# Performance work log

Hardware: AMD Instinct MI355X
Metric: run time of the kernel (lower is better)

The kernel has to match this reference:

```python
import jax, jax.numpy as jnp
import numpy as np

B, C, L = 32, 8, 2048
K, S = 512, 64  # num_shapelets, shapelets_size


def setup_inputs() -> dict:
    key = jax.random.key(0)
    k1, k2 = jax.random.split(key)
    x = jax.random.normal(k1, (B, C, L), dtype=jnp.float32)
    shapelets = jax.random.normal(k2, (C, K, S), dtype=jnp.float32)
    return {"x": x, "shapelets": shapelets}


def reference(x, shapelets):
    # x: [B, C, L]; shapelets: [C, K, S]
    s = shapelets.shape[-1]
    n_dims = x.shape[1]
    W = x.shape[2] - s + 1  # number of sliding windows
    # unfold(2, S, 1): gather overlapping windows -> [B, C, W, S]
    idx = jnp.arange(W)[:, None] + jnp.arange(s)[None, :]
    xw = x[:, :, idx]
    # L2-normalize windows along window length (clamp min like torch)
    xw = xw / jnp.maximum(jnp.linalg.norm(xw, axis=-1, keepdims=True), 1e-8)
    # L2-normalize shapelets along length
    sn = shapelets / jnp.maximum(jnp.linalg.norm(shapelets, axis=-1, keepdims=True), 1e-8)
    # matmul [B,C,W,S] @ [C,S,K] then sum over C, fused into one einsum -> [B, W, K]
    sim = jnp.einsum('bcws,cks->bwk', xw, sn) / n_dims
    sim = jax.nn.relu(sim)
    # max over window positions -> [B, K]; keep the singleton channel dim like torch ([B,1,K])
    out = jnp.max(sim, axis=1)
    return out[:, None, :]
```

## Files before the change

### kernel.cpp

```cpp
#include <hip/hip_runtime.h>


#define B_ 32
#define C_ 8
#define L_ 2048
#define K_ 512
#define S_ 64
#define W_ 1985
#define XS_ 2176

typedef _Float16 f16x8  __attribute__((ext_vector_type(8)));
typedef _Float16 f16x8u __attribute__((ext_vector_type(8), aligned(4)));
typedef float    f32x16 __attribute__((ext_vector_type(16)));

__global__ __launch_bounds__(256)
void prep_k(const float* __restrict__ x, const float* __restrict__ sh,
            _Float16* __restrict__ Bp, float* __restrict__ invn,
            _Float16* __restrict__ xh0, _Float16* __restrict__ xh1,
            float* __restrict__ out) {
    __shared__ float xr[L_];
    const int tid = threadIdx.x;
    const int blk = blockIdx.x;

    if (blk < 128) {
        const int sb   = blk * 4 + (tid >> 6);
        const int c    = sb >> 6;
        const int kq   = (sb >> 4) & 3;
        const int nt   = sb & 15;
        const int lane = tid & 63;
        const int half = lane >> 5;
        const int q    = nt * 32 + (lane & 31);

        const float4* sp = (const float4*)(sh + (size_t)(c * K_ + q) * S_);
        float ss = 0.f;
        #pragma unroll
        for (int i = 0; i < 8; ++i) {
            float4 v = sp[half * 8 + i];
            ss += v.x * v.x + v.y * v.y + v.z * v.z + v.w * v.w;
        }
        ss += __shfl_xor(ss, 32);
        float inv = 1.f / fmaxf(sqrtf(ss), 1e-8f);

        float4 u0 = sp[kq * 4 + half * 2];
        float4 u1 = sp[kq * 4 + half * 2 + 1];
        f16x8 o;
        o[0] = (_Float16)(u0.x * inv); o[1] = (_Float16)(u0.y * inv);
        o[2] = (_Float16)(u0.z * inv); o[3] = (_Float16)(u0.w * inv);
        o[4] = (_Float16)(u1.x * inv); o[5] = (_Float16)(u1.y * inv);
        o[6] = (_Float16)(u1.z * inv); o[7] = (_Float16)(u1.w * inv);
        ((f16x8*)Bp)[((c * 4 + kq) * 16 + nt) * 64 + lane] = o;
    } else {
        const int r = blk - 128;
        const float* xp = x + (size_t)r * L_;
        for (int i = tid; i < L_ / 4; i += 256)
            ((float4*)xr)[i] = ((const float4*)xp)[i];
        __syncthreads();

        float* ivp = invn + (size_t)r * L_;
        const int w0 = tid * 8;
        float ss = 0.f;
        if (w0 < W_) {
            #pragma unroll
            for (int j = 0; j < S_; ++j) { float v = xr[w0 + j]; ss += v * v; }
        }
        #pragma unroll
        for (int u = 0; u < 8; ++u) {
            int w = w0 + u;
            float o = 0.f;
            if (u > 0 && w < W_)
                ss += xr[w + 63] * xr[w + 63] - xr[w - 1] * xr[w - 1];
            if (w < W_) o = 0.125f / fmaxf(sqrtf(ss), 1e-8f);
            if (w < L_) ivp[w] = o;
        }

        _Float16* p0 = xh0 + (size_t)r * XS_;
        _Float16* p1 = xh1 + (size_t)r * XS_;
        for (int i = tid; i < XS_ / 8; i += 256) {
            f16x8 o0, o1;
            #pragma unroll
            for (int j = 0; j < 8; ++j) {
                int e = i * 8 + j;
                o0[j] = (_Float16)((e     < L_) ? xr[e]     : 0.f);
                o1[j] = (_Float16)((e + 1 < L_) ? xr[e + 1] : 0.f);
            }
            ((f16x8*)p0)[i] = o0;
            ((f16x8*)p1)[i] = o1;
        }
        if (r < 64) out[r * 256 + tid] = 0.f;
    }
}

__device__ __forceinline__ void load_c(
    int c, const f16x8* __restrict__ bpbase, const _Float16* __restrict__ xbase,
    const float* __restrict__ ivbase, int m0, int m1,
    f16x8 (&bf)[8], f16x8 (&ar)[8], float (&iv)[2])
{
    iv[0] = ivbase[(size_t)c * L_ + m0];
    iv[1] = ivbase[(size_t)c * L_ + m1];
    #pragma unroll
    for (int ks = 0; ks < 4; ++ks)
        #pragma unroll
        for (int nt = 0; nt < 2; ++nt)
            bf[ks * 2 + nt] = bpbase[((c * 4 + ks) * 16 + nt) * 64];
    const _Float16* xp = xbase + (size_t)c * XS_;
    #pragma unroll
    for (int mt = 0; mt < 2; ++mt)
        #pragma unroll
        for (int ks = 0; ks < 4; ++ks)
            ar[mt * 4 + ks] = *(const f16x8u*)(xp + mt * 32 + ks * 16);
}

__device__ __forceinline__ void comp_c(
    const f16x8 (&bf)[8], const f16x8 (&ar)[8], const float (&iv)[2],
    f32x16 (&acc)[2][2])
{
    const _Float16 h0 = (_Float16)iv[0], h1 = (_Float16)iv[1];
    f16x8 is0, is1;
    #pragma unroll
    for (int j = 0; j < 8; ++j) { is0[j] = h0; is1[j] = h1; }
    #pragma unroll
    for (int ks = 0; ks < 4; ++ks) {
        f16x8 a0 = ar[0 * 4 + ks] * is0;
        f16x8 a1 = ar[1 * 4 + ks] * is1;
        #pragma unroll
        for (int nt = 0; nt < 2; ++nt) {
            acc[0][nt] = __builtin_amdgcn_mfma_f32_32x32x16_f16(
                a0, bf[ks * 2 + nt], acc[0][nt], 0, 0, 0);
            acc[1][nt] = __builtin_amdgcn_mfma_f32_32x32x16_f16(
                a1, bf[ks * 2 + nt], acc[1][nt], 0, 0, 0);
        }
    }
}

__global__ __launch_bounds__(256, 2)
void mcs_k(const _Float16* __restrict__ xh0, const _Float16* __restrict__ xh1,
           const _Float16* __restrict__ Bp, const float* __restrict__ invn,
           float* __restrict__ out) {
    const int wt  = blockIdx.x;
    const int ng  = blockIdx.y;
    const int b   = blockIdx.z;
    const int tid = threadIdx.x;
    const int lane = tid & 63;
    const int wv   = tid >> 6;
    const int mg   = wv >> 1;
    const int nw   = wv & 1;

    const int l31 = lane & 31;
    const int lh  = lane >> 5;
    const int Wb  = wt * 128 + mg * 64;
    const int m0  = Wb + l31;
    const int m1  = Wb + 32 + l31;

    const _Float16* xb = (l31 & 1) ? (xh1 - 1) : xh0;
    const _Float16* xbase = xb + (size_t)b * C_ * XS_ + Wb + l31 + lh * 8;
    const float*   ivbase = invn + (size_t)b * C_ * L_;
    const f16x8*   bpbase = (const f16x8*)Bp + (ng * 4 + nw * 2) * 64 + lane;

    f32x16 acc[2][2];
    #pragma unroll
    for (int mt = 0; mt < 2; ++mt)
        #pragma unroll
        for (int nt = 0; nt < 2; ++nt)
            #pragma unroll
            for (int r = 0; r < 16; ++r) acc[mt][nt][r] = 0.f;

    f16x8 bA[8], aA[8], bB[8], aB[8];
    float ivA[2], ivB[2];

    load_c(0, bpbase, xbase, ivbase, m0, m1, bA, aA, ivA);
    #pragma unroll 1
    for (int cp = 0; cp < 4; ++cp) {
        const int c0 = cp * 2;
        load_c(c0 + 1, bpbase, xbase, ivbase, m0, m1, bB, aB, ivB);
        comp_c(bA, aA, ivA, acc);
        if (cp < 3)
            load_c(c0 + 2, bpbase, xbase, ivbase, m0, m1, bA, aA, ivA);
        comp_c(bB, aB, ivB, acc);
    }

    float m[2];
    #pragma unroll
    for (int nt = 0; nt < 2; ++nt) {
        float v = 0.f;
        #pragma unroll
        for (int mt = 0; mt < 2; ++mt)
            #pragma unroll
            for (int r = 0; r < 16; ++r) v = fmaxf(v, acc[mt][nt][r]);
        v = fmaxf(v, __shfl_xor(v, 32));
        m[nt] = v;
    }

    __shared__ float red[2][2][32];
    if (mg == 0 && lane < 32) {
        red[nw][0][l31] = m[0];
        red[nw][1][l31] = m[1];
    }
    __syncthreads();
    if (mg == 1 && lane < 32) {
        #pragma unroll
        for (int nt = 0; nt < 2; ++nt) {
            float v = fmaxf(m[nt], red[nw][nt][l31]);
            atomicMax((unsigned int*)(out + (size_t)b * K_ + ng * 128 + nw * 64 + nt * 32 + l31),
                      __float_as_uint(v));
        }
    }
}

extern "C" void kernel_launch(void* const* d_in, const int* in_sizes, int n_in,
                              void* d_out, int out_size, void* d_ws, size_t ws_size,
                              hipStream_t stream) {
    const float* x  = (const float*)d_in[0];
    const float* sh = (const float*)d_in[1];
    float* out = (float*)d_out;

    _Float16* Bp   = (_Float16*)d_ws;
    float*    invn = (float*)((char*)d_ws + (512 << 10));
    _Float16* xh0  = (_Float16*)((char*)d_ws + (512 << 10) + (2 << 20));
    _Float16* xh1  = xh0 + (size_t)B_ * C_ * XS_;

    prep_k<<<dim3(384), dim3(256), 0, stream>>>(x, sh, Bp, invn, xh0, xh1, out);
    mcs_k<<<dim3(16, 4, B_), dim3(256), 0, stream>>>(xh0, xh1, Bp, invn, out);
}
```

Baseline: 104.0 us.

## Stage shapelet fragments into LDS via direct global-to-LDS loads shared across waves

Shapelet B fragments for each channel are no longer loaded per wave straight into registers. Each wave now issues 16-byte global_load_lds copies for one quarter of the fragments into a double-buffered shared array. All waves then read their B operands from LDS, so the two M-groups no longer fetch the same data from global memory twice, and B register pressure drops. The cost is two block-wide barriers per channel pair and extra LDS reads. Correctness depends on the barrier waiting for the asynchronous LDS writes to finish.

```diff
diff --git a/kernel.cpp b/kernel.cpp
--- a/kernel.cpp
+++ b/kernel.cpp
@@ -90,18 +90,18 @@
     }
 }
 
-__device__ __forceinline__ void load_c(
-    int c, const f16x8* __restrict__ bpbase, const _Float16* __restrict__ xbase,
-    const float* __restrict__ ivbase, int m0, int m1,
-    f16x8 (&bf)[8], f16x8 (&ar)[8], float (&iv)[2])
+__device__ __forceinline__ void glds16(const void* g, void* l) {
+    __builtin_amdgcn_global_load_lds(
+        (const __attribute__((address_space(1))) unsigned int*)g,
+        (__attribute__((address_space(3))) unsigned int*)l, 16, 0, 0);
+}
+
+__device__ __forceinline__ void loadA(
+    int c, const _Float16* __restrict__ xbase, const float* __restrict__ ivbase,
+    int m0, int m1, f16x8 (&ar)[8], float (&iv)[2])
 {
     iv[0] = ivbase[(size_t)c * L_ + m0];
     iv[1] = ivbase[(size_t)c * L_ + m1];
-    #pragma unroll
-    for (int ks = 0; ks < 4; ++ks)
-        #pragma unroll
-        for (int nt = 0; nt < 2; ++nt)
-            bf[ks * 2 + nt] = bpbase[((c * 4 + ks) * 16 + nt) * 64];
     const _Float16* xp = xbase + (size_t)c * XS_;
     #pragma unroll
     for (int mt = 0; mt < 2; ++mt)
@@ -110,14 +110,22 @@
             ar[mt * 4 + ks] = *(const f16x8u*)(xp + mt * 32 + ks * 16);
 }
 
-__device__ __forceinline__ void comp_c(
-    const f16x8 (&bf)[8], const f16x8 (&ar)[8], const float (&iv)[2],
-    f32x16 (&acc)[2][2])
+__device__ __forceinline__ void compC(
+    const f16x8* __restrict__ bsl, int lane, int nw,
+    const f16x8 (&ar)[8], const float (&iv)[2], f32x16 (&acc)[2][2])
 {
+    f16x8 bf[8];
+    #pragma unroll
+    for (int ks = 0; ks < 4; ++ks)
+        #pragma unroll
+        for (int nt = 0; nt < 2; ++nt)
+            bf[ks * 2 + nt] = bsl[(ks * 4 + nw * 2 + nt) * 64 + lane];
+
     const _Float16 h0 = (_Float16)iv[0], h1 = (_Float16)iv[1];
     f16x8 is0, is1;
     #pragma unroll
     for (int j = 0; j < 8; ++j) { is0[j] = h0; is1[j] = h1; }
+
     #pragma unroll
     for (int ks = 0; ks < 4; ++ks) {
         f16x8 a0 = ar[0 * 4 + ks] * is0;
@@ -151,10 +159,13 @@
     const int m0  = Wb + l31;
     const int m1  = Wb + 32 + l31;
 
+    __shared__ f16x8 Bs[2][16][64];
+    __shared__ float red[2][2][32];
+
     const _Float16* xb = (l31 & 1) ? (xh1 - 1) : xh0;
     const _Float16* xbase = xb + (size_t)b * C_ * XS_ + Wb + l31 + lh * 8;
     const float*   ivbase = invn + (size_t)b * C_ * L_;
-    const f16x8*   bpbase = (const f16x8*)Bp + (ng * 4 + nw * 2) * 64 + lane;
+    const f16x8*   sg = (const f16x8*)Bp + ((wv * 16 + ng * 4) * 64) + lane;
 
     f32x16 acc[2][2];
     #pragma unroll
@@ -164,19 +175,33 @@
             #pragma unroll
             for (int r = 0; r < 16; ++r) acc[mt][nt][r] = 0.f;
 
-    f16x8 bA[8], aA[8], bB[8], aB[8];
+    f16x8 aA[8], aB[8];
     float ivA[2], ivB[2];
 
-    load_c(0, bpbase, xbase, ivbase, m0, m1, bA, aA, ivA);
+    #define STAGE(c, buf)                                              \
+        { _Pragma("unroll")                                            \
+          for (int u = 0; u < 4; ++u)                                  \
+              glds16(sg + ((c) * 64 + u) * 64, &Bs[buf][wv * 4 + u][0]); }
+
+    STAGE(0, 0);
+    loadA(0, xbase, ivbase, m0, m1, aA, ivA);
+    __syncthreads();
+
     #pragma unroll 1
     for (int cp = 0; cp < 4; ++cp) {
         const int c0 = cp * 2;
-        load_c(c0 + 1, bpbase, xbase, ivbase, m0, m1, bB, aB, ivB);
-        comp_c(bA, aA, ivA, acc);
-        if (cp < 3)
-            load_c(c0 + 2, bpbase, xbase, ivbase, m0, m1, bA, aA, ivA);
-        comp_c(bB, aB, ivB, acc);
-    }
+        STAGE(c0 + 1, 1);
+        loadA(c0 + 1, xbase, ivbase, m0, m1, aB, ivB);
+        compC(&Bs[0][0][0], lane, nw, aA, ivA, acc);
+        __syncthreads();
+        if (cp < 3) {
+            STAGE(c0 + 2, 0);
+            loadA(c0 + 2, xbase, ivbase, m0, m1, aA, ivA);
+        }
+        compC(&Bs[1][0][0], lane, nw, aB, ivB, acc);
+        __syncthreads();
+    }
+    #undef STAGE
 
     float m[2];
     #pragma unroll
@@ -190,7 +215,6 @@
         m[nt] = v;
     }
 
-    __shared__ float red[2][2][32];
     if (mg == 0 && lane < 32) {
         red[nw][0][l31] = m[0];
         red[nw][1][l31] = m[1];
```

After: 99.50 us. -4.3%, faster.
